# Kernel tuning notes

Measured on AMD Instinct MI355X. Metric: run time of the kernel, lower is better.

The kernel has to match this reference:

```python
import jax, jax.numpy as jnp
import numpy as np

N, E, D, H, F = 50000, 800000, 256, 4, 32
NEG_SLOPE = 0.2

def setup_inputs() -> dict:
    key = jax.random.key(0)
    ks = jax.random.split(key, 8)
    h = jax.random.normal(ks[0], (N, D), dtype=jnp.float32)
    W = jax.random.normal(ks[1], (D, H * F), dtype=jnp.float32) * (1.0 / np.sqrt(D))
    attn_l_w = jax.random.normal(ks[2], (F, 1), dtype=jnp.float32) * (1.0 / np.sqrt(F))
    attn_l_b = jnp.zeros((1,), dtype=jnp.float32)
    attn_r_w = jax.random.normal(ks[3], (F, 1), dtype=jnp.float32) * (1.0 / np.sqrt(F))
    attn_r_b = jnp.zeros((1,), dtype=jnp.float32)
    bias = jnp.zeros((H, F), dtype=jnp.float32)
    src = jax.random.randint(ks[4], (E,), 0, N, dtype=jnp.int32)
    dst = jax.random.randint(ks[5], (E,), 0, N, dtype=jnp.int32)
    return {"h": h, "W": W, "attn_l_w": attn_l_w, "attn_l_b": attn_l_b,
            "attn_r_w": attn_r_w, "attn_r_b": attn_r_b, "bias": bias,
            "src": src, "dst": dst}

def reference(h, W, attn_l_w, attn_l_b, attn_r_w, attn_r_b, bias, src, dst):
    # node projection: [N, D] @ [D, H*F] -> [N, H, F]
    hW = (h @ W).reshape(N, H, F)
    # per-node attention halves: Dense(1) over F -> [N, H, 1]
    el = jnp.einsum('nhf,fo->nho', hW, attn_l_w) + attn_l_b
    er = jnp.einsum('nhf,fo->nho', hW, attn_r_w) + attn_r_b
    # edge logits: src contributes er, dst contributes el -> [E, H, 1]
    e = er[src] + el[dst]
    e = jnp.where(e >= 0, e, NEG_SLOPE * e)  # leaky_relu
    # segment softmax over destination groups
    emax = jax.ops.segment_max(e, dst, num_segments=N)  # [N, H, 1]
    ee = jnp.exp(e - emax[dst])
    denom = jax.ops.segment_sum(ee, dst, num_segments=N)  # [N, H, 1]
    a = ee / denom[dst]  # [E, H, 1]
    # weighted message scatter-sum: [E, H, F] -> [N, H, F]
    m = hW[src] * a
    out = jax.ops.segment_sum(m, dst, num_segments=N) + bias
    return out
```

## Files before the change

### kernel.cpp

```cpp
#include <hip/hip_runtime.h>
#include <hip/hip_bf16.h>

#define N_NODES 50000
#define E_EDGES 800000
#define D_IN    256
#define H_HEADS 4
#define HF      128
#define NEG_SLOPE 0.2f
#define SCAN_BLOCKS ((N_NODES + 255) / 256)

typedef __attribute__((ext_vector_type(8))) short bf16x8;
typedef __attribute__((ext_vector_type(4))) float f32x4;

__global__ __launch_bounds__(256) void k_prepW(const float* __restrict__ W,
                                               __hip_bfloat16* __restrict__ Wt) {
    const int g = blockIdx.x * 256 + threadIdx.x;
    const int n = g >> 8;
    const int k = g & 255;
    Wt[n * D_IN + k] = __float2bfloat16(W[k * HF + n]);
}

__global__ __launch_bounds__(256) void k_gemm(const float* __restrict__ h,
                                              const __hip_bfloat16* __restrict__ Wt,
                                              const float* __restrict__ lw,
                                              const float* __restrict__ lb,
                                              const float* __restrict__ rw,
                                              const float* __restrict__ rb,
                                              __hip_bfloat16* __restrict__ hW,
                                              float* __restrict__ el,
                                              float* __restrict__ er) {
    __shared__ __hip_bfloat16 As[64][72];
    __shared__ __hip_bfloat16 Bs[128][72];
    const int t    = threadIdx.x;
    const int r0   = blockIdx.x * 64;
    const int wave = t >> 6;
    const int lane = t & 63;
    const int l16  = lane & 15;
    const int quad = lane >> 4;

    f32x4 acc[8] = {};

    for (int k0 = 0; k0 < D_IN; k0 += 64) {
        {
            const int row  = t >> 2;
            const int koff = (t & 3) * 16;
            const int n    = r0 + row;
            float v[16];
            if (n < N_NODES) {
                const float* p = h + (size_t)n * D_IN + k0 + koff;
                *(float4*)&v[0]  = ((const float4*)p)[0];
                *(float4*)&v[4]  = ((const float4*)p)[1];
                *(float4*)&v[8]  = ((const float4*)p)[2];
                *(float4*)&v[12] = ((const float4*)p)[3];
            } else {
                #pragma unroll
                for (int i = 0; i < 16; ++i) v[i] = 0.f;
            }
            __hip_bfloat16 b[16];
            #pragma unroll
            for (int i = 0; i < 16; ++i) b[i] = __float2bfloat16(v[i]);
            *(uint4*)&As[row][koff]     = ((uint4*)b)[0];
            *(uint4*)&As[row][koff + 8] = ((uint4*)b)[1];
        }
        {
            const int n    = t >> 1;
            const int koff = (t & 1) * 32;
            const uint4* p = (const uint4*)(Wt + n * D_IN + k0 + koff);
            uint4 b0 = p[0], b1 = p[1], b2 = p[2], b3 = p[3];
            uint4* q = (uint4*)&Bs[n][koff];
            q[0] = b0; q[1] = b1; q[2] = b2; q[3] = b3;
        }
        __syncthreads();

        #pragma unroll
        for (int ks = 0; ks < 2; ++ks) {
            const bf16x8 af = *(const bf16x8*)&As[wave * 16 + l16][ks * 32 + quad * 8];
            #pragma unroll
            for (int nt = 0; nt < 8; ++nt) {
                const bf16x8 bfg = *(const bf16x8*)&Bs[nt * 16 + l16][ks * 32 + quad * 8];
                acc[nt] = __builtin_amdgcn_mfma_f32_16x16x32_bf16(af, bfg, acc[nt], 0, 0, 0);
            }
        }
        __syncthreads();
    }

    const int mbase = r0 + wave * 16 + quad * 4;
    #pragma unroll
    for (int nt = 0; nt < 8; ++nt) {
        #pragma unroll
        for (int r = 0; r < 4; ++r) {
            const int m = mbase + r;
            if (m < N_NODES)
                hW[(size_t)m * HF + nt * 16 + l16] = __float2bfloat16(acc[nt][r]);
        }
    }

    const float lwv0 = lw[l16], lwv1 = lw[l16 + 16];
    const float rwv0 = rw[l16], rwv1 = rw[l16 + 16];
    const float lb0 = lb[0], rb0 = rb[0];
    #pragma unroll
    for (int r = 0; r < 4; ++r) {
        const int m = mbase + r;
        float el4[4], er4[4];
        #pragma unroll
        for (int hh = 0; hh < 4; ++hh) {
            float pl = acc[2 * hh][r] * lwv0 + acc[2 * hh + 1][r] * lwv1;
            float pr = acc[2 * hh][r] * rwv0 + acc[2 * hh + 1][r] * rwv1;
            #pragma unroll
            for (int o = 1; o < 16; o <<= 1) {
                pl += __shfl_xor(pl, o);
                pr += __shfl_xor(pr, o);
            }
            el4[hh] = pl + lb0;
            er4[hh] = pr + rb0;
        }
        if (l16 == 0 && m < N_NODES) {
            *(float4*)&el[m * H_HEADS] = make_float4(el4[0], el4[1], el4[2], el4[3]);
            *(float4*)&er[m * H_HEADS] = make_float4(er4[0], er4[1], er4[2], er4[3]);
        }
    }
}

__global__ __launch_bounds__(256) void k_hist(const int* __restrict__ dst,
                                              unsigned* __restrict__ cnt) {
    const int g = blockIdx.x * 256 + threadIdx.x;
    atomicAdd(&cnt[dst[g]], 1u);
}

__global__ __launch_bounds__(256) void k_scan(const unsigned* __restrict__ cnt,
                                              unsigned* __restrict__ off) {
    __shared__ unsigned s[256];
    const int t = threadIdx.x;
    const int b = blockIdx.x;
    const int base = b * 256;

    unsigned part = 0;
    #pragma unroll 4
    for (int i = t; i < base; i += 256) part += cnt[i];
    s[t] = part;
    __syncthreads();
    #pragma unroll
    for (int o = 128; o > 0; o >>= 1) {
        if (t < o) s[t] += s[t + o];
        __syncthreads();
    }
    const unsigned pre = s[0];
    __syncthreads();

    const int g = base + t;
    const unsigned x = (g < N_NODES) ? cnt[g] : 0u;
    s[t] = x;
    __syncthreads();
    unsigned inc = x;
    #pragma unroll
    for (int o = 1; o < 256; o <<= 1) {
        const unsigned v = (t >= o) ? s[t - o] : 0u;
        __syncthreads();
        inc += v;
        s[t] = inc;
        __syncthreads();
    }
    if (g < N_NODES) off[g] = pre + inc - x;
}

__global__ __launch_bounds__(256) void k_fill(const int* __restrict__ src,
                                              const int* __restrict__ dst,
                                              unsigned* __restrict__ off,
                                              unsigned* __restrict__ perm) {
    const int g = blockIdx.x * 256 + threadIdx.x;
    const unsigned p = atomicAdd(&off[dst[g]], 1u);
    perm[p] = (unsigned)src[g];
}

__global__ __launch_bounds__(256) void k_aggregate(const __hip_bfloat16* __restrict__ hW,
                                                   const float* __restrict__ el,
                                                   const float* __restrict__ er,
                                                   const unsigned* __restrict__ off_end,
                                                   const unsigned* __restrict__ perm,
                                                   const float* __restrict__ bias,
                                                   float* __restrict__ out) {
    const int wave = threadIdx.x >> 6;
    const int lane = threadIdx.x & 63;
    const int n    = blockIdx.x * 4 + wave;
    const int hh   = lane >> 4;
    const unsigned beg = (n == 0) ? 0u : off_end[n - 1];
    const unsigned end = off_end[n];
    const float eld = el[n * H_HEADS + hh];
    const unsigned* hWu = (const unsigned*)hW;

    float a0 = 0.f, a1 = 0.f, denom = 0.f;
    unsigned j = beg;
    for (; j + 4 <= end; j += 4) {
        int s[4];
        #pragma unroll
        for (int u = 0; u < 4; ++u) s[u] = (int)perm[j + u];
        unsigned g2[4];
        float e4[4];
        #pragma unroll
        for (int u = 0; u < 4; ++u) {
            g2[u] = hWu[(size_t)s[u] * (HF / 2) + lane];
            e4[u] = er[s[u] * H_HEADS + hh];
        }
        #pragma unroll
        for (int u = 0; u < 4; ++u) {
            float v = e4[u] + eld;
            v = (v >= 0.f) ? v : NEG_SLOPE * v;
            const float p = __expf(v);
            denom += p;
            a0 += p * __uint_as_float(g2[u] << 16);
            a1 += p * __uint_as_float(g2[u] & 0xFFFF0000u);
        }
    }
    for (; j < end; ++j) {
        const int si = (int)perm[j];
        const unsigned g2 = hWu[(size_t)si * (HF / 2) + lane];
        float v = er[si * H_HEADS + hh] + eld;
        v = (v >= 0.f) ? v : NEG_SLOPE * v;
        const float p = __expf(v);
        denom += p;
        a0 += p * __uint_as_float(g2 << 16);
        a1 += p * __uint_as_float(g2 & 0xFFFF0000u);
    }
    const float inv = (end > beg) ? 1.f / denom : 0.f;
    const float2 bv = *(const float2*)&bias[lane * 2];
    float2 o2 = make_float2(a0 * inv + bv.x, a1 * inv + bv.y);
    *(float2*)&out[(size_t)n * HF + lane * 2] = o2;
}

extern "C" void kernel_launch(void* const* d_in, const int* in_sizes, int n_in,
                              void* d_out, int out_size, void* d_ws, size_t ws_size,
                              hipStream_t stream) {
    const float* h    = (const float*)d_in[0];
    const float* W    = (const float*)d_in[1];
    const float* lw   = (const float*)d_in[2];
    const float* lb   = (const float*)d_in[3];
    const float* rw   = (const float*)d_in[4];
    const float* rb   = (const float*)d_in[5];
    const float* bias = (const float*)d_in[6];
    const int*   src  = (const int*)d_in[7];
    const int*   dst  = (const int*)d_in[8];
    float* out = (float*)d_out;

    float*    ws   = (float*)d_ws;
    float*    el   = ws;
    float*    er   = ws + 200000;
    unsigned* cnt  = (unsigned*)(ws + 400000);
    unsigned* off  = (unsigned*)(ws + 450000);
    unsigned* perm = (unsigned*)(ws + 500000);
    __hip_bfloat16* Wt = (__hip_bfloat16*)(ws + 1300000);
    __hip_bfloat16* hW = (__hip_bfloat16*)(ws + 1320000);

    hipMemsetAsync(cnt, 0, N_NODES * sizeof(unsigned), stream);
    k_prepW<<<128, 256, 0, stream>>>(W, Wt);
    k_gemm<<<(N_NODES + 63) / 64, 256, 0, stream>>>(h, Wt, lw, lb, rw, rb, hW, el, er);
    k_hist<<<E_EDGES / 256, 256, 0, stream>>>(dst, cnt);
    k_scan<<<SCAN_BLOCKS, 256, 0, stream>>>(cnt, off);
    k_fill<<<E_EDGES / 256, 256, 0, stream>>>(src, dst, off, perm);
    k_aggregate<<<N_NODES / 4, 256, 0, stream>>>(hW, el, er, off, perm, bias, out);
}
```

Before: 262.0 us.

## Merge independent launches: fuse histogram with W prep, and fill with GEMM

Combines independent kernels into horizontally fused launches that branch on block index. The histogram runs alongside the W transpose, and the CSR fill runs alongside the projection GEMM, so launch count drops from six to four and the atomic-bound fill can overlap the compute-bound GEMM. The cost is that fill blocks now reserve the GEMM's shared memory, which may reduce occupancy for the fill portion.

```diff
diff --git a/kernel.cpp b/kernel.cpp
--- a/kernel.cpp
+++ b/kernel.cpp
@@ -8,31 +8,91 @@
 #define HF      128
 #define NEG_SLOPE 0.2f
 #define SCAN_BLOCKS ((N_NODES + 255) / 256)
+#define HIST_BLOCKS (E_EDGES / 256)
+#define PREP_BLOCKS 128
+#define FILL_BLOCKS (E_EDGES / 256)
+#define GEMM_BLOCKS ((N_NODES + 63) / 64)
 
 typedef __attribute__((ext_vector_type(8))) short bf16x8;
 typedef __attribute__((ext_vector_type(4))) float f32x4;
 
-__global__ __launch_bounds__(256) void k_prepW(const float* __restrict__ W,
-                                               __hip_bfloat16* __restrict__ Wt) {
-    const int g = blockIdx.x * 256 + threadIdx.x;
-    const int n = g >> 8;
-    const int k = g & 255;
-    Wt[n * D_IN + k] = __float2bfloat16(W[k * HF + n]);
-}
-
-__global__ __launch_bounds__(256) void k_gemm(const float* __restrict__ h,
-                                              const __hip_bfloat16* __restrict__ Wt,
-                                              const float* __restrict__ lw,
-                                              const float* __restrict__ lb,
-                                              const float* __restrict__ rw,
-                                              const float* __restrict__ rb,
-                                              __hip_bfloat16* __restrict__ hW,
-                                              float* __restrict__ el,
-                                              float* __restrict__ er) {
+__global__ __launch_bounds__(256) void k_hist_prep(const int* __restrict__ dst,
+                                                   unsigned* __restrict__ cnt,
+                                                   const float* __restrict__ W,
+                                                   __hip_bfloat16* __restrict__ Wt) {
+    const int b = blockIdx.x;
+    if (b < HIST_BLOCKS) {
+        const int g = b * 256 + threadIdx.x;
+        atomicAdd(&cnt[dst[g]], 1u);
+    } else {
+        const int g = (b - HIST_BLOCKS) * 256 + threadIdx.x;
+        const int n = g >> 8;
+        const int k = g & 255;
+        Wt[n * D_IN + k] = __float2bfloat16(W[k * HF + n]);
+    }
+}
+
+__global__ __launch_bounds__(256) void k_scan(const unsigned* __restrict__ cnt,
+                                              unsigned* __restrict__ off) {
+    __shared__ unsigned s[256];
+    const int t = threadIdx.x;
+    const int b = blockIdx.x;
+    const int base = b * 256;
+
+    unsigned part = 0;
+    #pragma unroll 4
+    for (int i = t; i < base; i += 256) part += cnt[i];
+    s[t] = part;
+    __syncthreads();
+    #pragma unroll
+    for (int o = 128; o > 0; o >>= 1) {
+        if (t < o) s[t] += s[t + o];
+        __syncthreads();
+    }
+    const unsigned pre = s[0];
+    __syncthreads();
+
+    const int g = base + t;
+    const unsigned x = (g < N_NODES) ? cnt[g] : 0u;
+    s[t] = x;
+    __syncthreads();
+    unsigned inc = x;
+    #pragma unroll
+    for (int o = 1; o < 256; o <<= 1) {
+        const unsigned v = (t >= o) ? s[t - o] : 0u;
+        __syncthreads();
+        inc += v;
+        s[t] = inc;
+        __syncthreads();
+    }
+    if (g < N_NODES) off[g] = pre + inc - x;
+}
+
+__global__ __launch_bounds__(256) void k_fill_gemm(const int* __restrict__ src,
+                                                   const int* __restrict__ dst,
+                                                   unsigned* __restrict__ off,
+                                                   unsigned* __restrict__ perm,
+                                                   const float* __restrict__ h,
+                                                   const __hip_bfloat16* __restrict__ Wt,
+                                                   const float* __restrict__ lw,
+                                                   const float* __restrict__ lb,
+                                                   const float* __restrict__ rw,
+                                                   const float* __restrict__ rb,
+                                                   __hip_bfloat16* __restrict__ hW,
+                                                   float* __restrict__ el,
+                                                   float* __restrict__ er) {
     __shared__ __hip_bfloat16 As[64][72];
     __shared__ __hip_bfloat16 Bs[128][72];
+
+    if (blockIdx.x < FILL_BLOCKS) {
+        const int g = blockIdx.x * 256 + threadIdx.x;
+        const unsigned p = atomicAdd(&off[dst[g]], 1u);
+        perm[p] = (unsigned)src[g];
+        return;
+    }
+
     const int t    = threadIdx.x;
-    const int r0   = blockIdx.x * 64;
+    const int r0   = (blockIdx.x - FILL_BLOCKS) * 64;
     const int wave = t >> 6;
     const int lane = t & 63;
     const int l16  = lane & 15;
@@ -121,57 +181,6 @@
     }
 }
 
-__global__ __launch_bounds__(256) void k_hist(const int* __restrict__ dst,
-                                              unsigned* __restrict__ cnt) {
-    const int g = blockIdx.x * 256 + threadIdx.x;
-    atomicAdd(&cnt[dst[g]], 1u);
-}
-
-__global__ __launch_bounds__(256) void k_scan(const unsigned* __restrict__ cnt,
-                                              unsigned* __restrict__ off) {
-    __shared__ unsigned s[256];
-    const int t = threadIdx.x;
-    const int b = blockIdx.x;
-    const int base = b * 256;
-
-    unsigned part = 0;
-    #pragma unroll 4
-    for (int i = t; i < base; i += 256) part += cnt[i];
-    s[t] = part;
-    __syncthreads();
-    #pragma unroll
-    for (int o = 128; o > 0; o >>= 1) {
-        if (t < o) s[t] += s[t + o];
-        __syncthreads();
-    }
-    const unsigned pre = s[0];
-    __syncthreads();
-
-    const int g = base + t;
-    const unsigned x = (g < N_NODES) ? cnt[g] : 0u;
-    s[t] = x;
-    __syncthreads();
-    unsigned inc = x;
-    #pragma unroll
-    for (int o = 1; o < 256; o <<= 1) {
-        const unsigned v = (t >= o) ? s[t - o] : 0u;
-        __syncthreads();
-        inc += v;
-        s[t] = inc;
-        __syncthreads();
-    }
-    if (g < N_NODES) off[g] = pre + inc - x;
-}
-
-__global__ __launch_bounds__(256) void k_fill(const int* __restrict__ src,
-                                              const int* __restrict__ dst,
-                                              unsigned* __restrict__ off,
-                                              unsigned* __restrict__ perm) {
-    const int g = blockIdx.x * 256 + threadIdx.x;
-    const unsigned p = atomicAdd(&off[dst[g]], 1u);
-    perm[p] = (unsigned)src[g];
-}
-
 __global__ __launch_bounds__(256) void k_aggregate(const __hip_bfloat16* __restrict__ hW,
                                                    const float* __restrict__ el,
                                                    const float* __restrict__ er,
@@ -251,10 +260,9 @@
     __hip_bfloat16* hW = (__hip_bfloat16*)(ws + 1320000);
 
     hipMemsetAsync(cnt, 0, N_NODES * sizeof(unsigned), stream);
-    k_prepW<<<128, 256, 0, stream>>>(W, Wt);
-    k_gemm<<<(N_NODES + 63) / 64, 256, 0, stream>>>(h, Wt, lw, lb, rw, rb, hW, el, er);
-    k_hist<<<E_EDGES / 256, 256, 0, stream>>>(dst, cnt);
+    k_hist_prep<<<HIST_BLOCKS + PREP_BLOCKS, 256, 0, stream>>>(dst, cnt, W, Wt);
     k_scan<<<SCAN_BLOCKS, 256, 0, stream>>>(cnt, off);
-    k_fill<<<E_EDGES / 256, 256, 0, stream>>>(src, dst, off, perm);
+    k_fill_gemm<<<FILL_BLOCKS + GEMM_BLOCKS, 256, 0, stream>>>(
+        src, dst, off, perm, h, Wt, lw, lb, rw, rb, hW, el, er);
     k_aggregate<<<N_NODES / 4, 256, 0, stream>>>(hW, el, er, off, perm, bias, out);
 }
```

Result: no change. 263.8 us (+0.7%).
